# Performance work log

Hardware: AMD Instinct MI355X
Metric: run time of the kernel (lower is better)

The kernel has to match this reference:

```python
import jax, jax.numpy as jnp
import numpy as np

B, N, D, E, H = 16, 256, 64, 64, 8


def setup_inputs() -> dict:
    key = jax.random.key(0)
    ks = jax.random.split(key, 16)
    s = 0.05
    return {
        "query": jax.random.normal(ks[0], (B, N, D), jnp.float32),
        "edges_augmented": jax.random.normal(ks[1], (B, N, N, E), jnp.float32),
        "Wq": jax.random.normal(ks[2], (D, H * D), jnp.float32) * s,
        "bq": jnp.zeros((H * D,), jnp.float32),
        "Wk": jax.random.normal(ks[3], (D, H * D), jnp.float32) * s,
        "bk": jnp.zeros((H * D,), jnp.float32),
        "Wv": jax.random.normal(ks[4], (D, H * D), jnp.float32) * s,
        "bv": jnp.zeros((H * D,), jnp.float32),
        "Wa": jax.random.normal(ks[5], (E, H), jnp.float32) * s,
        "ba": jnp.zeros((H,), jnp.float32),
        "Wg": jax.random.normal(ks[6], (E, H), jnp.float32) * s,
        "bg": jnp.zeros((H,), jnp.float32),
        "Wo": jax.random.normal(ks[7], (H * D, D), jnp.float32) * s,
        "bo": jnp.zeros((D,), jnp.float32),
        "We": jax.random.normal(ks[8], (H, E), jnp.float32) * s,
        "be": jnp.zeros((E,), jnp.float32),
    }


def reference(query, edges_augmented, Wq, bq, Wk, bk, Wv, bv, Wa, ba, Wg, bg, Wo, bo, We, be):
    b, n, d = query.shape
    h = Wa.shape[1]
    # QKV projections -> [b, h, n, d]
    Q = (query @ Wq + bq).reshape(b, n, h, d).transpose(0, 2, 1, 3)
    Kt = (query @ Wk + bk).reshape(b, n, h, d).transpose(0, 2, 1, 3)
    V = (query @ Wv + bv).reshape(b, n, h, d).transpose(0, 2, 1, 3)
    scores = jnp.einsum('bhnd,bhmd->bhnm', Q, Kt) / jnp.sqrt(jnp.asarray(d, query.dtype))
    # edge-derived additive bias: [b,n,n,h] -> [b,h,n,n]
    attn_bias = (edges_augmented @ Wa + ba).transpose(0, 3, 1, 2)
    scores = scores + attn_bias
    # sigmoid gate on values
    g = jax.nn.sigmoid((edges_augmented @ Wg + bg).transpose(0, 3, 1, 2))  # [b,h,n,n]
    Vg = jnp.einsum('bhnm,bhmd->bhnd', g, V)
    attn = jax.nn.softmax(scores, axis=-1)
    out = jnp.einsum('bhnm,bhmd->bhnd', attn, Vg)
    out = out.transpose(0, 2, 1, 3).reshape(b, n, h * d)
    attention_output = out @ Wo + bo  # [b, n, d]
    # edges output: scores [b,h,n,m] -> [b,m,n,h] -> Dense to E
    edges_output = scores.transpose(0, 3, 2, 1) @ We + be  # [b, n, n, E]
    return (attention_output, edges_output)
```

## Files before the change

### kernel.cpp

```cpp
#include <hip/hip_runtime.h>

#define BB 16
#define NN 256
#define DD 64
#define EE 64
#define HH 8

__device__ __forceinline__ void fma4(float* acc, float x, float4 w) {
    acc[0] += x * w.x; acc[1] += x * w.y; acc[2] += x * w.z; acc[3] += x * w.w;
}

__global__ __launch_bounds__(256) void qkv_kernel(
    const float* __restrict__ query,
    const float* __restrict__ Wq, const float* __restrict__ bq,
    const float* __restrict__ Wk, const float* __restrict__ bk,
    const float* __restrict__ Wv, const float* __restrict__ bv,
    float* __restrict__ Qt, float* __restrict__ Kt, float* __restrict__ V)
{
    __shared__ __align__(16) float q_l[8][64];
    const int mtx = blockIdx.x >> 9;
    const int rem = blockIdx.x & 511;
    const int b   = rem >> 5;
    const int n0  = (rem & 31) << 3;
    const int tid = threadIdx.x;

    if (tid < 128)
        ((float4*)&q_l[0][0])[tid] =
            ((const float4*)(query + (size_t)(b * NN + n0) * DD))[tid];

    const int w    = tid >> 6;
    const int lane = tid & 63;
    const int r0   = w * 2;
    const float* W  = (mtx == 0) ? Wq : (mtx == 1) ? Wk : Wv;
    const float* bs = (mtx == 0) ? bq : (mtx == 1) ? bk : bv;

    const int c0 = lane << 2;
    float acc[2][2][4];
    {
        const float4 b0 = *(const float4*)(bs + c0);
        const float4 b1 = *(const float4*)(bs + 256 + c0);
        acc[0][0][0]=b0.x; acc[0][0][1]=b0.y; acc[0][0][2]=b0.z; acc[0][0][3]=b0.w;
        acc[0][1][0]=b1.x; acc[0][1][1]=b1.y; acc[0][1][2]=b1.z; acc[0][1][3]=b1.w;
        acc[1][0][0]=b0.x; acc[1][0][1]=b0.y; acc[1][0][2]=b0.z; acc[1][0][3]=b0.w;
        acc[1][1][0]=b1.x; acc[1][1][1]=b1.y; acc[1][1][2]=b1.z; acc[1][1][3]=b1.w;
    }
    __syncthreads();

    #pragma unroll 2
    for (int d4 = 0; d4 < 16; ++d4) {
        const float4 qa = ((const float4*)&q_l[r0][0])[d4];
        const float4 qb = ((const float4*)&q_l[r0 + 1][0])[d4];
        const float qav[4] = {qa.x, qa.y, qa.z, qa.w};
        const float qbv[4] = {qb.x, qb.y, qb.z, qb.w};
        #pragma unroll
        for (int k = 0; k < 4; ++k) {
            const float4 w0 = *(const float4*)(W + (size_t)(d4 * 4 + k) * 512 + c0);
            const float4 w1 = *(const float4*)(W + (size_t)(d4 * 4 + k) * 512 + 256 + c0);
            fma4(acc[0][0], qav[k], w0); fma4(acc[0][1], qav[k], w1);
            fma4(acc[1][0], qbv[k], w0); fma4(acc[1][1], qbv[k], w1);
        }
    }

    const int hq = lane >> 4;
    const int d0 = (lane & 15) << 2;
    if (mtx == 2) {
        #pragma unroll
        for (int r = 0; r < 2; ++r)
            #pragma unroll
            for (int j = 0; j < 2; ++j) {
                const int h = j * 4 + hq;
                *(float4*)(V + (size_t)((b * HH + h) * NN + n0 + r0 + r) * DD + d0) =
                    make_float4(acc[r][j][0], acc[r][j][1], acc[r][j][2], acc[r][j][3]);
            }
    } else {
        float* T = (mtx == 0) ? Qt : Kt;
        #pragma unroll
        for (int r = 0; r < 2; ++r)
            #pragma unroll
            for (int j = 0; j < 2; ++j) {
                const int h = j * 4 + hq;
                #pragma unroll
                for (int k = 0; k < 4; ++k)
                    T[(size_t)((b * HH + h) * DD + d0 + k) * NN + n0 + r0 + r] =
                        acc[r][j][k];
            }
    }
}

__global__ __launch_bounds__(256) void qk_kernel(
    const float* __restrict__ Qt, const float* __restrict__ Kt,
    float* __restrict__ scores)
{
    __shared__ __align__(16) float qt_l[64][64];
    __shared__ __align__(16) float kt_l[64][64];
    const int mt  = blockIdx.x & 3;
    const int nt  = (blockIdx.x >> 2) & 3;
    const int bh  = blockIdx.x >> 4;
    const int n0  = nt << 6, m0 = mt << 6;
    const int tid = threadIdx.x;

    {
        const int dr = tid >> 4;
        const int c4 = (tid & 15) << 2;
        const float* qsrc = Qt + (size_t)bh * 64 * 256 + n0;
        const float* ksrc = Kt + (size_t)bh * 64 * 256 + m0;
        #pragma unroll
        for (int it = 0; it < 4; ++it) {
            const int d = it * 16 + dr;
            *(float4*)&qt_l[d][c4] = *(const float4*)(qsrc + d * 256 + c4);
            *(float4*)&kt_l[d][c4] = *(const float4*)(ksrc + d * 256 + c4);
        }
    }
    __syncthreads();

    const int tx = tid & 15, ty = tid >> 4;
    float acc[4][4] = {};
    #pragma unroll 8
    for (int d = 0; d < 64; ++d) {
        const float4 q4 = *(const float4*)&qt_l[d][ty << 2];
        const float4 k4 = *(const float4*)&kt_l[d][tx << 2];
        const float qa[4] = {q4.x, q4.y, q4.z, q4.w};
        #pragma unroll
        for (int i = 0; i < 4; ++i)
            fma4(acc[i], qa[i], k4);
    }
    float* sp = scores + ((size_t)bh * 256 + n0 + (ty << 2)) * 256 + m0 + (tx << 2);
    #pragma unroll
    for (int i = 0; i < 4; ++i)
        *(float4*)(sp + i * 256) =
            make_float4(acc[i][0] * 0.125f, acc[i][1] * 0.125f,
                        acc[i][2] * 0.125f, acc[i][3] * 0.125f);
}

__global__ __launch_bounds__(256) void edges_kernel(
    const float* __restrict__ edges,
    const float* __restrict__ Wa, const float* __restrict__ ba,
    const float* __restrict__ Wg, const float* __restrict__ bg,
    const float* __restrict__ We, const float* __restrict__ be,
    float* __restrict__ scores,
    float* __restrict__ gates,
    float* __restrict__ edges_out)
{
    __shared__ __align__(16) float wa_l[EE * HH];
    __shared__ __align__(16) float wg_l[EE * HH];
    __shared__ float ba_l[HH], bg_l[HH];
    __shared__ __align__(16) float sc_l[4][64][HH];

    const int mt   = blockIdx.x & 3;
    const int nt   = (blockIdx.x >> 2) & 63;
    const int b    = blockIdx.x >> 8;
    const int n0   = nt << 2;
    const int m0   = mt << 6;
    const int tid  = threadIdx.x;
    const int lane = tid & 63;
    const int np   = tid >> 6;
    const int mp   = lane;

    for (int i = tid; i < 512; i += 256) { wa_l[i] = Wa[i]; wg_l[i] = Wg[i]; }
    if (tid < 8) { ba_l[tid] = ba[tid]; bg_l[tid] = bg[tid]; }

    float wecol[8];
    #pragma unroll
    for (int h = 0; h < 8; ++h) wecol[h] = We[h * EE + lane];
    const float bev = be[lane];

    const size_t so = (size_t)b * HH * NN * NN + (size_t)(n0 + np) * NN + m0 + mp;
    float qk[8];
    #pragma unroll
    for (int h = 0; h < 8; ++h) qk[h] = scores[so + (size_t)h * NN * NN];

    const float4* ep = (const float4*)(edges +
                        (size_t)((b * NN + n0 + np) * NN + m0 + mp) * DD);
    float4 xr[16];
    #pragma unroll
    for (int i = 0; i < 16; ++i) xr[i] = ep[i];

    __syncthreads();

    float bias[8], gate[8];
    #pragma unroll
    for (int h = 0; h < 8; ++h) { bias[h] = ba_l[h]; gate[h] = bg_l[h]; }
    #pragma unroll
    for (int e4 = 0; e4 < 16; ++e4) {
        const float xs[4] = {xr[e4].x, xr[e4].y, xr[e4].z, xr[e4].w};
        #pragma unroll
        for (int k = 0; k < 4; ++k) {
            const int e = e4 * 4 + k;
            const float4 wa0 = *(const float4*)&wa_l[e * 8];
            const float4 wa1 = *(const float4*)&wa_l[e * 8 + 4];
            const float4 wg0 = *(const float4*)&wg_l[e * 8];
            const float4 wg1 = *(const float4*)&wg_l[e * 8 + 4];
            fma4(&bias[0], xs[k], wa0); fma4(&bias[4], xs[k], wa1);
            fma4(&gate[0], xs[k], wg0); fma4(&gate[4], xs[k], wg1);
        }
    }

    float sc[8], gg[8];
    #pragma unroll
    for (int h = 0; h < 8; ++h) {
        sc[h] = qk[h] + bias[h];
        gg[h] = 1.f / (1.f + __expf(-gate[h]));
    }
    #pragma unroll
    for (int h = 0; h < 8; ++h) {
        scores[so + (size_t)h * NN * NN] = sc[h];
        gates [so + (size_t)h * NN * NN] = gg[h];
    }
    *(float4*)&sc_l[np][mp][0] = make_float4(sc[0], sc[1], sc[2], sc[3]);
    *(float4*)&sc_l[np][mp][4] = make_float4(sc[4], sc[5], sc[6], sc[7]);
    __syncthreads();

    #pragma unroll 8
    for (int pi = 0; pi < 64; ++pi) {
        const int p   = np * 64 + pi;
        const int mp2 = p >> 2, np2 = p & 3;
        const float4 sa = *(const float4*)&sc_l[np2][mp2][0];
        const float4 sb = *(const float4*)&sc_l[np2][mp2][4];
        const float v = bev
            + sa.x * wecol[0] + sa.y * wecol[1] + sa.z * wecol[2] + sa.w * wecol[3]
            + sb.x * wecol[4] + sb.y * wecol[5] + sb.z * wecol[6] + sb.w * wecol[7];
        edges_out[(size_t)((b * NN + m0 + mp2) * NN + n0 + np2) * DD + lane] = v;
    }
}

__global__ __launch_bounds__(256) void vg_kernel(
    const float* __restrict__ gates, const float* __restrict__ V,
    float* __restrict__ Vg)
{
    __shared__ __align__(16) float g_l[16][256];
    const int bh  = blockIdx.x >> 4;
    const int n0  = (blockIdx.x & 15) << 4;
    const int tid = threadIdx.x;

    const float4* gsrc = (const float4*)(gates + (size_t)bh * NN * NN + (size_t)n0 * NN);
    #pragma unroll
    for (int i = 0; i < 4; ++i)
        ((float4*)&g_l[0][0])[tid + i * 256] = gsrc[tid + i * 256];
    __syncthreads();

    const int wv   = tid >> 6;
    const int msub = (tid >> 4) & 3;
    const int dq   = tid & 15;
    float acc[4][4] = {};
    const float* vb = V + (size_t)bh * NN * DD + dq * 4;
    #pragma unroll 4
    for (int mq = 0; mq < 64; ++mq) {
        const int m = mq * 4 + msub;
        const float4 v4 = *(const float4*)(vb + m * DD);
        #pragma unroll
        for (int i = 0; i < 4; ++i) {
            const float a = g_l[wv * 4 + i][m];
            acc[i][0] += a * v4.x; acc[i][1] += a * v4.y;
            acc[i][2] += a * v4.z; acc[i][3] += a * v4.w;
        }
    }
    #pragma unroll
    for (int i = 0; i < 4; ++i) {
        #pragma unroll
        for (int c = 0; c < 4; ++c) {
            acc[i][c] += __shfl_xor(acc[i][c], 16, 64);
            acc[i][c] += __shfl_xor(acc[i][c], 32, 64);
        }
        if (msub == 0)
            *(float4*)(Vg + (size_t)(bh * NN + n0 + wv * 4 + i) * DD + dq * 4) =
                make_float4(acc[i][0], acc[i][1], acc[i][2], acc[i][3]);
    }
}

__global__ __launch_bounds__(512) void out_kernel(
    const float* __restrict__ scores, const float* __restrict__ Vg,
    const float* __restrict__ Wo, const float* __restrict__ bo,
    float* __restrict__ att_out)
{
    __shared__ __align__(16) float att_l[8][256];
    __shared__ __align__(16) float o_l[8][512];
    const int b    = blockIdx.x >> 5;
    const int n0   = (blockIdx.x & 31) << 3;
    const int tid  = threadIdx.x;
    const int np   = tid >> 6;
    const int lane = tid & 63;
    const int msub = (lane >> 4) & 3;
    const int dq   = lane & 15;

    for (int h = 0; h < 8; ++h) {
        const float* sp = scores + (size_t)((b * HH + h) * NN + n0 + np) * NN;
        const float4 s4 = ((const float4*)sp)[lane];
        float mx = fmaxf(fmaxf(s4.x, s4.y), fmaxf(s4.z, s4.w));
        #pragma unroll
        for (int off = 32; off; off >>= 1) mx = fmaxf(mx, __shfl_xor(mx, off, 64));
        const float e0 = __expf(s4.x - mx), e1 = __expf(s4.y - mx),
                    e2 = __expf(s4.z - mx), e3 = __expf(s4.w - mx);
        float sm = e0 + e1 + e2 + e3;
        #pragma unroll
        for (int off = 32; off; off >>= 1) sm += __shfl_xor(sm, off, 64);
        const float inv = 1.f / sm;
        ((float4*)&att_l[np][0])[lane] = make_float4(e0 * inv, e1 * inv, e2 * inv, e3 * inv);

        float a0 = 0.f, a1 = 0.f, a2 = 0.f, a3 = 0.f;
        const float* vb = Vg + (size_t)((b * HH + h) * NN) * DD + dq * 4;
        #pragma unroll 4
        for (int mq = 0; mq < 64; ++mq) {
            const int m = mq * 4 + msub;
            const float a = att_l[np][m];
            const float4 v4 = *(const float4*)(vb + m * DD);
            a0 += a * v4.x; a1 += a * v4.y; a2 += a * v4.z; a3 += a * v4.w;
        }
        a0 += __shfl_xor(a0, 16, 64); a0 += __shfl_xor(a0, 32, 64);
        a1 += __shfl_xor(a1, 16, 64); a1 += __shfl_xor(a1, 32, 64);
        a2 += __shfl_xor(a2, 16, 64); a2 += __shfl_xor(a2, 32, 64);
        a3 += __shfl_xor(a3, 16, 64); a3 += __shfl_xor(a3, 32, 64);
        if (msub == 0)
            *(float4*)&o_l[np][h * 64 + dq * 4] = make_float4(a0, a1, a2, a3);
    }

    float acc = bo[lane];
    const float*  wp   = Wo + lane;
    const float4* orow = (const float4*)&o_l[np][0];
    #pragma unroll 4
    for (int k4 = 0; k4 < 128; ++k4) {
        const float4 o4 = orow[k4];
        acc += o4.x * wp[(k4 * 4 + 0) * 64] + o4.y * wp[(k4 * 4 + 1) * 64]
             + o4.z * wp[(k4 * 4 + 2) * 64] + o4.w * wp[(k4 * 4 + 3) * 64];
    }
    att_out[(size_t)(b * NN + n0 + np) * DD + lane] = acc;
}

extern "C" void kernel_launch(void* const* d_in, const int* in_sizes, int n_in,
                              void* d_out, int out_size, void* d_ws, size_t ws_size,
                              hipStream_t stream)
{
    const float* query = (const float*)d_in[0];
    const float* edges = (const float*)d_in[1];
    const float* Wq = (const float*)d_in[2];  const float* bq = (const float*)d_in[3];
    const float* Wk = (const float*)d_in[4];  const float* bk = (const float*)d_in[5];
    const float* Wv = (const float*)d_in[6];  const float* bv = (const float*)d_in[7];
    const float* Wa = (const float*)d_in[8];  const float* ba = (const float*)d_in[9];
    const float* Wg = (const float*)d_in[10]; const float* bg = (const float*)d_in[11];
    const float* Wo = (const float*)d_in[12]; const float* bo = (const float*)d_in[13];
    const float* We = (const float*)d_in[14]; const float* be = (const float*)d_in[15];

    float* att_out   = (float*)d_out;
    float* edges_out = (float*)d_out + 262144;

    float* ws     = (float*)d_ws;
    float* Qt     = ws;
    float* Kt     = ws + 2097152;
    float* V      = ws + 4194304;
    float* Vg     = ws + 6291456;
    float* gates  = ws + 8388608;
    float* scores = ws + 16777216;

    hipLaunchKernelGGL(qkv_kernel, dim3(1536), dim3(256), 0, stream,
                       query, Wq, bq, Wk, bk, Wv, bv, Qt, Kt, V);
    hipLaunchKernelGGL(qk_kernel, dim3(2048), dim3(256), 0, stream,
                       Qt, Kt, scores);
    hipLaunchKernelGGL(edges_kernel, dim3(4096), dim3(256), 0, stream,
                       edges, Wa, ba, Wg, bg, We, be, scores, gates, edges_out);
    hipLaunchKernelGGL(vg_kernel, dim3(2048), dim3(256), 0, stream,
                       gates, V, Vg);
    hipLaunchKernelGGL(out_kernel, dim3(512), dim3(512), 0, stream,
                       scores, Vg, Wo, bo, att_out);
}
```

Before: 689.3 us.

## Use bf16 MFMA for QK, gated-V and attention-V matmuls with bf16 intermediates

```diff
diff --git a/kernel.cpp b/kernel.cpp
--- a/kernel.cpp
+++ b/kernel.cpp
@@ -6,8 +6,17 @@
 #define EE 64
 #define HH 8
 
+typedef __attribute__((ext_vector_type(4))) float f32x4;
+typedef __attribute__((ext_vector_type(8))) short short8;
+
 __device__ __forceinline__ void fma4(float* acc, float x, float4 w) {
     acc[0] += x * w.x; acc[1] += x * w.y; acc[2] += x * w.z; acc[3] += x * w.w;
+}
+
+__device__ __forceinline__ unsigned short f2bf(float f) {
+    union { float f; unsigned u; } v; v.f = f;
+    unsigned r = v.u + 0x7FFFu + ((v.u >> 16) & 1u);
+    return (unsigned short)(r >> 16);
 }
 
 __global__ __launch_bounds__(256) void qkv_kernel(
@@ -15,7 +24,8 @@
     const float* __restrict__ Wq, const float* __restrict__ bq,
     const float* __restrict__ Wk, const float* __restrict__ bk,
     const float* __restrict__ Wv, const float* __restrict__ bv,
-    float* __restrict__ Qt, float* __restrict__ Kt, float* __restrict__ V)
+    unsigned short* __restrict__ Qb, unsigned short* __restrict__ Kb,
+    unsigned short* __restrict__ Vtb)
 {
     __shared__ __align__(16) float q_l[8][64];
     const int mtx = blockIdx.x >> 9;
@@ -63,17 +73,22 @@
 
     const int hq = lane >> 4;
     const int d0 = (lane & 15) << 2;
-    if (mtx == 2) {
+    if (mtx < 2) {
+        unsigned short* T = (mtx == 0) ? Qb : Kb;
+        const float scale = (mtx == 0) ? 0.125f : 1.0f;
         #pragma unroll
         for (int r = 0; r < 2; ++r)
             #pragma unroll
             for (int j = 0; j < 2; ++j) {
                 const int h = j * 4 + hq;
-                *(float4*)(V + (size_t)((b * HH + h) * NN + n0 + r0 + r) * DD + d0) =
-                    make_float4(acc[r][j][0], acc[r][j][1], acc[r][j][2], acc[r][j][3]);
+                const unsigned int lo = (unsigned)f2bf(acc[r][j][0] * scale)
+                                      | ((unsigned)f2bf(acc[r][j][1] * scale) << 16);
+                const unsigned int hi = (unsigned)f2bf(acc[r][j][2] * scale)
+                                      | ((unsigned)f2bf(acc[r][j][3] * scale) << 16);
+                uint2* p = (uint2*)(T + ((size_t)(b * HH + h) * NN + n0 + r0 + r) * DD + d0);
+                *p = make_uint2(lo, hi);
             }
     } else {
-        float* T = (mtx == 0) ? Qt : Kt;
         #pragma unroll
         for (int r = 0; r < 2; ++r)
             #pragma unroll
@@ -81,55 +96,48 @@
                 const int h = j * 4 + hq;
                 #pragma unroll
                 for (int k = 0; k < 4; ++k)
-                    T[(size_t)((b * HH + h) * DD + d0 + k) * NN + n0 + r0 + r] =
-                        acc[r][j][k];
+                    Vtb[((size_t)(b * HH + h) * DD + d0 + k) * NN + n0 + r0 + r] =
+                        f2bf(acc[r][j][k]);
             }
     }
 }
 
 __global__ __launch_bounds__(256) void qk_kernel(
-    const float* __restrict__ Qt, const float* __restrict__ Kt,
+    const unsigned short* __restrict__ Qb, const unsigned short* __restrict__ Kb,
     float* __restrict__ scores)
 {
-    __shared__ __align__(16) float qt_l[64][64];
-    __shared__ __align__(16) float kt_l[64][64];
-    const int mt  = blockIdx.x & 3;
-    const int nt  = (blockIdx.x >> 2) & 3;
-    const int bh  = blockIdx.x >> 4;
-    const int n0  = nt << 6, m0 = mt << 6;
+    const int bh = blockIdx.x >> 3;
+    const int nt = (blockIdx.x >> 1) & 3;
+    const int mh = blockIdx.x & 1;
     const int tid = threadIdx.x;
-
-    {
-        const int dr = tid >> 4;
-        const int c4 = (tid & 15) << 2;
-        const float* qsrc = Qt + (size_t)bh * 64 * 256 + n0;
-        const float* ksrc = Kt + (size_t)bh * 64 * 256 + m0;
-        #pragma unroll
-        for (int it = 0; it < 4; ++it) {
-            const int d = it * 16 + dr;
-            *(float4*)&qt_l[d][c4] = *(const float4*)(qsrc + d * 256 + c4);
-            *(float4*)&kt_l[d][c4] = *(const float4*)(ksrc + d * 256 + c4);
-        }
-    }
-    __syncthreads();
-
-    const int tx = tid & 15, ty = tid >> 4;
-    float acc[4][4] = {};
-    #pragma unroll 8
-    for (int d = 0; d < 64; ++d) {
-        const float4 q4 = *(const float4*)&qt_l[d][ty << 2];
-        const float4 k4 = *(const float4*)&kt_l[d][tx << 2];
-        const float qa[4] = {q4.x, q4.y, q4.z, q4.w};
-        #pragma unroll
-        for (int i = 0; i < 4; ++i)
-            fma4(acc[i], qa[i], k4);
-    }
-    float* sp = scores + ((size_t)bh * 256 + n0 + (ty << 2)) * 256 + m0 + (tx << 2);
-    #pragma unroll
-    for (int i = 0; i < 4; ++i)
-        *(float4*)(sp + i * 256) =
-            make_float4(acc[i][0] * 0.125f, acc[i][1] * 0.125f,
-                        acc[i][2] * 0.125f, acc[i][3] * 0.125f);
+    const int w = tid >> 6, l = tid & 63;
+    const int lr = l & 15, lg = l >> 4;
+    const int n0 = nt * 64 + w * 16;
+
+    const unsigned short* qp = Qb + ((size_t)bh * NN + n0 + lr) * DD + lg * 8;
+    const unsigned short* kp = Kb + ((size_t)bh * NN + mh * 128 + lr) * DD + lg * 8;
+
+    const short8 a0 = *(const short8*)qp;
+    const short8 a1 = *(const short8*)(qp + 32);
+
+    f32x4 acc[8];
+    #pragma unroll
+    for (int mt = 0; mt < 8; ++mt) acc[mt] = (f32x4){0.f, 0.f, 0.f, 0.f};
+
+    #pragma unroll
+    for (int mt = 0; mt < 8; ++mt) {
+        const short8 b0 = *(const short8*)(kp + (size_t)mt * 16 * DD);
+        const short8 b1 = *(const short8*)(kp + (size_t)mt * 16 * DD + 32);
+        acc[mt] = __builtin_amdgcn_mfma_f32_16x16x32_bf16(a0, b0, acc[mt], 0, 0, 0);
+        acc[mt] = __builtin_amdgcn_mfma_f32_16x16x32_bf16(a1, b1, acc[mt], 0, 0, 0);
+    }
+
+    float* sp = scores + (size_t)bh * NN * NN;
+    #pragma unroll
+    for (int mt = 0; mt < 8; ++mt)
+        #pragma unroll
+        for (int r = 0; r < 4; ++r)
+            sp[(size_t)(n0 + lg * 4 + r) * NN + mh * 128 + mt * 16 + lr] = acc[mt][r];
 }
 
 __global__ __launch_bounds__(256) void edges_kernel(
@@ -138,7 +146,7 @@
     const float* __restrict__ Wg, const float* __restrict__ bg,
     const float* __restrict__ We, const float* __restrict__ be,
     float* __restrict__ scores,
-    float* __restrict__ gates,
+    unsigned short* __restrict__ gates,
     float* __restrict__ edges_out)
 {
     __shared__ __align__(16) float wa_l[EE * HH];
@@ -195,16 +203,13 @@
         }
     }
 
-    float sc[8], gg[8];
+    float sc[8];
     #pragma unroll
     for (int h = 0; h < 8; ++h) {
         sc[h] = qk[h] + bias[h];
-        gg[h] = 1.f / (1.f + __expf(-gate[h]));
-    }
-    #pragma unroll
-    for (int h = 0; h < 8; ++h) {
+        const float gg = 1.f / (1.f + __expf(-gate[h]));
         scores[so + (size_t)h * NN * NN] = sc[h];
-        gates [so + (size_t)h * NN * NN] = gg[h];
+        gates [so + (size_t)h * NN * NN] = f2bf(gg);
     }
     *(float4*)&sc_l[np][mp][0] = make_float4(sc[0], sc[1], sc[2], sc[3]);
     *(float4*)&sc_l[np][mp][4] = make_float4(sc[4], sc[5], sc[6], sc[7]);
@@ -224,105 +229,117 @@
 }
 
 __global__ __launch_bounds__(256) void vg_kernel(
-    const float* __restrict__ gates, const float* __restrict__ V,
-    float* __restrict__ Vg)
-{
-    __shared__ __align__(16) float g_l[16][256];
-    const int bh  = blockIdx.x >> 4;
-    const int n0  = (blockIdx.x & 15) << 4;
+    const unsigned short* __restrict__ gates, const unsigned short* __restrict__ Vtb,
+    unsigned short* __restrict__ Vgt)
+{
+    const int bh = blockIdx.x >> 2;
+    const int q  = blockIdx.x & 3;
     const int tid = threadIdx.x;
-
-    const float4* gsrc = (const float4*)(gates + (size_t)bh * NN * NN + (size_t)n0 * NN);
-    #pragma unroll
-    for (int i = 0; i < 4; ++i)
-        ((float4*)&g_l[0][0])[tid + i * 256] = gsrc[tid + i * 256];
-    __syncthreads();
-
-    const int wv   = tid >> 6;
-    const int msub = (tid >> 4) & 3;
-    const int dq   = tid & 15;
-    float acc[4][4] = {};
-    const float* vb = V + (size_t)bh * NN * DD + dq * 4;
-    #pragma unroll 4
-    for (int mq = 0; mq < 64; ++mq) {
-        const int m = mq * 4 + msub;
-        const float4 v4 = *(const float4*)(vb + m * DD);
-        #pragma unroll
-        for (int i = 0; i < 4; ++i) {
-            const float a = g_l[wv * 4 + i][m];
-            acc[i][0] += a * v4.x; acc[i][1] += a * v4.y;
-            acc[i][2] += a * v4.z; acc[i][3] += a * v4.w;
-        }
-    }
-    #pragma unroll
-    for (int i = 0; i < 4; ++i) {
-        #pragma unroll
-        for (int c = 0; c < 4; ++c) {
-            acc[i][c] += __shfl_xor(acc[i][c], 16, 64);
-            acc[i][c] += __shfl_xor(acc[i][c], 32, 64);
-        }
-        if (msub == 0)
-            *(float4*)(Vg + (size_t)(bh * NN + n0 + wv * 4 + i) * DD + dq * 4) =
-                make_float4(acc[i][0], acc[i][1], acc[i][2], acc[i][3]);
-    }
-}
-
-__global__ __launch_bounds__(512) void out_kernel(
-    const float* __restrict__ scores, const float* __restrict__ Vg,
+    const int w = tid >> 6, l = tid & 63;
+    const int lr = l & 15, lg = l >> 4;
+    const int n0 = q * 64 + w * 16;
+
+    const unsigned short* gp = gates + ((size_t)bh * NN + n0 + lr) * NN + lg * 8;
+    const unsigned short* vp = Vtb + ((size_t)bh * DD + lr) * NN + lg * 8;
+
+    f32x4 acc[4];
+    #pragma unroll
+    for (int dt = 0; dt < 4; ++dt) acc[dt] = (f32x4){0.f, 0.f, 0.f, 0.f};
+
+    #pragma unroll
+    for (int ks = 0; ks < 8; ++ks) {
+        const short8 bfr = *(const short8*)(gp + ks * 32);
+        #pragma unroll
+        for (int dt = 0; dt < 4; ++dt) {
+            const short8 afr = *(const short8*)(vp + (size_t)dt * 16 * NN + ks * 32);
+            acc[dt] = __builtin_amdgcn_mfma_f32_16x16x32_bf16(afr, bfr, acc[dt], 0, 0, 0);
+        }
+    }
+
+    unsigned short* op = Vgt + (size_t)bh * DD * NN;
+    #pragma unroll
+    for (int dt = 0; dt < 4; ++dt)
+        #pragma unroll
+        for (int r = 0; r < 4; ++r)
+            op[(size_t)(dt * 16 + lg * 4 + r) * NN + n0 + lr] = f2bf(acc[dt][r]);
+}
+
+__global__ __launch_bounds__(256) void out_kernel(
+    const float* __restrict__ scores, const unsigned short* __restrict__ Vgt,
     const float* __restrict__ Wo, const float* __restrict__ bo,
     float* __restrict__ att_out)
 {
-    __shared__ __align__(16) float att_l[8][256];
-    __shared__ __align__(16) float o_l[8][512];
-    const int b    = blockIdx.x >> 5;
-    const int n0   = (blockIdx.x & 31) << 3;
-    const int tid  = threadIdx.x;
-    const int np   = tid >> 6;
-    const int lane = tid & 63;
-    const int msub = (lane >> 4) & 3;
-    const int dq   = lane & 15;
-
-    for (int h = 0; h < 8; ++h) {
-        const float* sp = scores + (size_t)((b * HH + h) * NN + n0 + np) * NN;
-        const float4 s4 = ((const float4*)sp)[lane];
-        float mx = fmaxf(fmaxf(s4.x, s4.y), fmaxf(s4.z, s4.w));
-        #pragma unroll
-        for (int off = 32; off; off >>= 1) mx = fmaxf(mx, __shfl_xor(mx, off, 64));
-        const float e0 = __expf(s4.x - mx), e1 = __expf(s4.y - mx),
-                    e2 = __expf(s4.z - mx), e3 = __expf(s4.w - mx);
-        float sm = e0 + e1 + e2 + e3;
-        #pragma unroll
-        for (int off = 32; off; off >>= 1) sm += __shfl_xor(sm, off, 64);
+    __shared__ __align__(16) float o_l[16][513];
+    const int b  = blockIdx.x >> 4;
+    const int nt = blockIdx.x & 15;
+    const int n0 = nt * 16;
+    const int tid = threadIdx.x;
+    const int w = tid >> 6, l = tid & 63;
+    const int lr = l & 15, lg = l >> 4;
+
+    #pragma unroll
+    for (int hw = 0; hw < 2; ++hw) {
+        const int h = w + hw * 4;
+        const float* sp = scores + ((size_t)(b * HH + h) * NN + n0 + lr) * NN + lg * 8;
+
+        float s[64];
+        #pragma unroll
+        for (int ks = 0; ks < 8; ++ks) {
+            const float4 x0 = *(const float4*)(sp + ks * 32);
+            const float4 x1 = *(const float4*)(sp + ks * 32 + 4);
+            s[ks * 8 + 0] = x0.x; s[ks * 8 + 1] = x0.y;
+            s[ks * 8 + 2] = x0.z; s[ks * 8 + 3] = x0.w;
+            s[ks * 8 + 4] = x1.x; s[ks * 8 + 5] = x1.y;
+            s[ks * 8 + 6] = x1.z; s[ks * 8 + 7] = x1.w;
+        }
+        float mx = -1e30f;
+        #pragma unroll
+        for (int i = 0; i < 64; ++i) mx = fmaxf(mx, s[i]);
+        mx = fmaxf(mx, __shfl_xor(mx, 16, 64));
+        mx = fmaxf(mx, __shfl_xor(mx, 32, 64));
+        float sm = 0.f;
+        #pragma unroll
+        for (int i = 0; i < 64; ++i) { s[i] = __expf(s[i] - mx); sm += s[i]; }
+        sm += __shfl_xor(sm, 16, 64);
+        sm += __shfl_xor(sm, 32, 64);
         const float inv = 1.f / sm;
-        ((float4*)&att_l[np][0])[lane] = make_float4(e0 * inv, e1 * inv, e2 * inv, e3 * inv);
-
-        float a0 = 0.f, a1 = 0.f, a2 = 0.f, a3 = 0.f;
-        const float* vb = Vg + (size_t)((b * HH + h) * NN) * DD + dq * 4;
-        #pragma unroll 4
-        for (int mq = 0; mq < 64; ++mq) {
-            const int m = mq * 4 + msub;
-            const float a = att_l[np][m];
-            const float4 v4 = *(const float4*)(vb + m * DD);
-            a0 += a * v4.x; a1 += a * v4.y; a2 += a * v4.z; a3 += a * v4.w;
-        }
-        a0 += __shfl_xor(a0, 16, 64); a0 += __shfl_xor(a0, 32, 64);
-        a1 += __shfl_xor(a1, 16, 64); a1 += __shfl_xor(a1, 32, 64);
-        a2 += __shfl_xor(a2, 16, 64); a2 += __shfl_xor(a2, 32, 64);
-        a3 += __shfl_xor(a3, 16, 64); a3 += __shfl_xor(a3, 32, 64);
-        if (msub == 0)
-            *(float4*)&o_l[np][h * 64 + dq * 4] = make_float4(a0, a1, a2, a3);
-    }
-
-    float acc = bo[lane];
-    const float*  wp   = Wo + lane;
-    const float4* orow = (const float4*)&o_l[np][0];
-    #pragma unroll 4
-    for (int k4 = 0; k4 < 128; ++k4) {
-        const float4 o4 = orow[k4];
-        acc += o4.x * wp[(k4 * 4 + 0) * 64] + o4.y * wp[(k4 * 4 + 1) * 64]
-             + o4.z * wp[(k4 * 4 + 2) * 64] + o4.w * wp[(k4 * 4 + 3) * 64];
-    }
-    att_out[(size_t)(b * NN + n0 + np) * DD + lane] = acc;
+
+        const unsigned short* vp = Vgt + ((size_t)(b * HH + h) * DD + lr) * NN + lg * 8;
+        f32x4 acc[4];
+        #pragma unroll
+        for (int dt = 0; dt < 4; ++dt) acc[dt] = (f32x4){0.f, 0.f, 0.f, 0.f};
+
+        #pragma unroll
+        for (int ks = 0; ks < 8; ++ks) {
+            union { short8 v; unsigned short u[8]; } bf;
+            #pragma unroll
+            for (int j = 0; j < 8; ++j) bf.u[j] = f2bf(s[ks * 8 + j] * inv);
+            #pragma unroll
+            for (int dt = 0; dt < 4; ++dt) {
+                const short8 afr = *(const short8*)(vp + (size_t)dt * 16 * NN + ks * 32);
+                acc[dt] = __builtin_amdgcn_mfma_f32_16x16x32_bf16(afr, bf.v, acc[dt], 0, 0, 0);
+            }
+        }
+        #pragma unroll
+        for (int dt = 0; dt < 4; ++dt)
+            #pragma unroll
+            for (int r = 0; r < 4; ++r)
+                o_l[lr][h * 64 + dt * 16 + lg * 4 + r] = acc[dt][r];
+    }
+    __syncthreads();
+
+    const int n  = tid >> 4;
+    const int d4 = (tid & 15) << 2;
+    float a0 = bo[d4], a1 = bo[d4 + 1], a2 = bo[d4 + 2], a3 = bo[d4 + 3];
+    const float* orow = &o_l[n][0];
+    #pragma unroll 8
+    for (int k = 0; k < 512; ++k) {
+        const float o = orow[k];
+        const float4 w4 = *(const float4*)(Wo + (size_t)k * 64 + d4);
+        a0 += o * w4.x; a1 += o * w4.y; a2 += o * w4.z; a3 += o * w4.w;
+    }
+    *(float4*)(att_out + ((size_t)(b * NN + n0 + n)) * DD + d4) =
+        make_float4(a0, a1, a2, a3);
 }
 
 extern "C" void kernel_launch(void* const* d_in, const int* in_sizes, int n_in,
@@ -342,22 +359,22 @@
     float* att_out   = (float*)d_out;
     float* edges_out = (float*)d_out + 262144;
 
-    float* ws     = (float*)d_ws;
-    float* Qt     = ws;
-    float* Kt     = ws + 2097152;
-    float* V      = ws + 4194304;
-    float* Vg     = ws + 6291456;
-    float* gates  = ws + 8388608;
-    float* scores = ws + 16777216;
+    char* base = (char*)d_ws;
+    float*          scores = (float*)base;
+    unsigned short* gates  = (unsigned short*)(base + 33554432);
+    unsigned short* Qb     = (unsigned short*)(base + 50331648);
+    unsigned short* Kb     = (unsigned short*)(base + 54525952);
+    unsigned short* Vtb    = (unsigned short*)(base + 58720256);
+    unsigned short* Vgt    = (unsigned short*)(base + 62914560);
 
     hipLaunchKernelGGL(qkv_kernel, dim3(1536), dim3(256), 0, stream,
-                       query, Wq, bq, Wk, bk, Wv, bv, Qt, Kt, V);
-    hipLaunchKernelGGL(qk_kernel, dim3(2048), dim3(256), 0, stream,
-                       Qt, Kt, scores);
+                       query, Wq, bq, Wk, bk, Wv, bv, Qb, Kb, Vtb);
+    hipLaunchKernelGGL(qk_kernel, dim3(1024), dim3(256), 0, stream,
+                       Qb, Kb, scores);
     hipLaunchKernelGGL(edges_kernel, dim3(4096), dim3(256), 0, stream,
                        edges, Wa, ba, Wg, bg, We, be, scores, gates, edges_out);
-    hipLaunchKernelGGL(vg_kernel, dim3(2048), dim3(256), 0, stream,
-                       gates, V, Vg);
-    hipLaunchKernelGGL(out_kernel, dim3(512), dim3(512), 0, stream,
-                       scores, Vg, Wo, bo, att_out);
-}
+    hipLaunchKernelGGL(vg_kernel, dim3(512), dim3(256), 0, stream,
+                       gates, Vtb, Vgt);
+    hipLaunchKernelGGL(out_kernel, dim3(256), dim3(256), 0, stream,
+                       scores, Vgt, Wo, bo, att_out);
+}
```

After: 601.6 us. -12.7%, faster.
